# Performance work log

Measured on AMD Instinct MI355X. Metric: run time of the kernel, lower is better.

## Reference

```python
import jax, jax.numpy as jnp
import numpy as np

ALPHA = 0.2  # LeakyReLU negative slope
NEG_BIG = -9e15


def setup_inputs() -> dict:
    key = jax.random.key(0)
    k1, k2, k3, k4 = jax.random.split(key, 4)
    N, F_IN, F_OUT = 8192, 256, 128
    h = jax.random.normal(k1, (N, F_IN), dtype=jnp.float32)
    adj = jax.random.randint(k2, (N, N), 0, 2, dtype=jnp.int32)
    # xavier_uniform with gain=1.414
    def xavier(k, shape, gain=1.414):
        fan_in, fan_out = shape[0], shape[1]
        bound = gain * np.sqrt(6.0 / (fan_in + fan_out))
        return jax.random.uniform(k, shape, jnp.float32, -bound, bound)
    W = xavier(k3, (F_IN, F_OUT))
    a = xavier(k4, (2 * F_OUT, 1))
    return {"h": h, "adj": adj, "W": W, "a": a}


def reference(h, adj, W, a):
    # Wh: [N, F_out]
    Wh = h @ W
    F_out = W.shape[1]
    a1 = a[:F_out, 0]   # attends to source (row) node
    a2 = a[F_out:, 0]   # attends to target (col) node
    # Additive decomposition of concat([Wh_i, Wh_j]) @ a:
    # e[i, j] = leaky_relu(Wh_i . a1 + Wh_j . a2)
    f1 = Wh @ a1  # [N]
    f2 = Wh @ a2  # [N]
    e = jax.nn.leaky_relu(f1[:, None] + f2[None, :], negative_slope=ALPHA)  # [N, N]
    scores = jnp.where(adj > 0, e, jnp.float32(NEG_BIG))
    attention = jax.nn.softmax(scores, axis=1)
    # dropout is identity in eval mode (training=False)
    h_prime = attention @ Wh  # [N, F_out]
    return h_prime
```

## Files before the change

### kernel.cpp

```cpp
#include <hip/hip_runtime.h>


#define N_NODES 8192
#define F_IN 256
#define F_OUT 128
#define RPB 64
#define JCH 128
#define JSPLIT 4
#define JRANGE (N_NODES / JSPLIT)
#define NCH (JRANGE / JCH)

typedef _Float16 half8 __attribute__((ext_vector_type(8)));
typedef float floatx4 __attribute__((ext_vector_type(4)));
typedef float f32x4 __attribute__((ext_vector_type(4)));
typedef int i32x4 __attribute__((ext_vector_type(4)));

__device__ __align__(16) float g_Wh[N_NODES * F_OUT];
__device__ __align__(16) _Float16 g_WhT[(size_t)F_OUT * N_NODES];
__device__ __align__(16) float g_f1[N_NODES];
__device__ __align__(16) float g_f2[N_NODES];
__device__ __align__(16) float g_part[JSPLIT][N_NODES * F_OUT];
__device__ __align__(16) float g_spart[JSPLIT][N_NODES];

__global__ __launch_bounds__(256, 2) void wh_kernel(
    const float* __restrict__ h, const float* __restrict__ W) {
  __shared__ float hT[F_IN][20];
  const int t = threadIdx.x;
  const int i0 = blockIdx.x * 16;
  {
    const int row = t >> 4;
    const int fu = t & 15;
#pragma unroll
    for (int r = 0; r < 4; ++r) {
      const int ku = r * 16 + fu;
      const float4 v = *(const float4*)(h + (size_t)(i0 + row) * F_IN + ku * 4);
      hT[ku * 4 + 0][row] = v.x; hT[ku * 4 + 1][row] = v.y;
      hT[ku * 4 + 2][row] = v.z; hT[ku * 4 + 3][row] = v.w;
    }
  }
  __syncthreads();
  const int c = t & 127;
  const int rg = t >> 7;
  float acc[8];
#pragma unroll
  for (int r = 0; r < 8; ++r) acc[r] = 0.f;
#pragma unroll 8
  for (int k = 0; k < F_IN; ++k) {
    const float wv = W[k * F_OUT + c];
    const float4 x0 = *(const float4*)(&hT[k][rg * 8]);
    const float4 x1 = *(const float4*)(&hT[k][rg * 8 + 4]);
    acc[0] = fmaf(x0.x, wv, acc[0]); acc[1] = fmaf(x0.y, wv, acc[1]);
    acc[2] = fmaf(x0.z, wv, acc[2]); acc[3] = fmaf(x0.w, wv, acc[3]);
    acc[4] = fmaf(x1.x, wv, acc[4]); acc[5] = fmaf(x1.y, wv, acc[5]);
    acc[6] = fmaf(x1.z, wv, acc[6]); acc[7] = fmaf(x1.w, wv, acc[7]);
  }
#pragma unroll
  for (int r = 0; r < 8; ++r)
    g_Wh[(size_t)(i0 + rg * 8 + r) * F_OUT + c] = acc[r];
  union { _Float16 hh[8]; uint4 u4; } pk;
#pragma unroll
  for (int r = 0; r < 8; ++r) pk.hh[r] = (_Float16)acc[r];
  *(uint4*)(g_WhT + (size_t)c * N_NODES + i0 + rg * 8) = pk.u4;
}

__global__ __launch_bounds__(256) void f12_kernel(const float* __restrict__ a) {
  const int t = threadIdx.x;
  const int row = blockIdx.x * 2 + (t >> 7);
  const int c = t & 127;
  const float wh = g_Wh[(size_t)row * F_OUT + c];
  float p1 = wh * a[c];
  float p2 = wh * a[F_OUT + c];
  for (int o = 32; o > 0; o >>= 1) {
    p1 += __shfl_down(p1, o, 64);
    p2 += __shfl_down(p2, o, 64);
  }
  __shared__ float s1[4], s2[4];
  const int w = t >> 6;
  if ((t & 63) == 0) { s1[w] = p1; s2[w] = p2; }
  __syncthreads();
  if ((t & 127) == 0) {
    g_f1[row] = s1[w] + s1[w + 1];
    g_f2[row] = s2[w] + s2[w + 1];
  }
}

__device__ __forceinline__ float score_p(int a, float f2v, float f1r) {
  float s = f1r + f2v;
  s = fmaxf(s, 0.2f * s);
  float arg = (a > 0) ? fmaf(s, 1.44269504088896f, -16.0f) : -1.0e5f;
  return __builtin_amdgcn_exp2f(arg);
}

__global__ __launch_bounds__(256, 2) void gat_attn_kernel(const int* __restrict__ adj) {
  const int t = threadIdx.x;
  const int wave = t >> 6;
  const int lane = t & 63;
  const int mrow = lane & 15;
  const int quad = lane >> 4;
  const int i0 = blockIdx.x * RPB;
  const int js = blockIdx.y;
  const int jbase = js * JRANGE;
  const int jloc = wave * 32 + quad * 8;

  float f1r[4];
#pragma unroll
  for (int tl = 0; tl < 4; ++tl) f1r[tl] = g_f1[i0 + tl * 16 + mrow];

  half8 ones;
#pragma unroll
  for (int e = 0; e < 8; ++e) ones[e] = (_Float16)1;

  floatx4 acc[4][8];
  floatx4 asum[4];
#pragma unroll
  for (int tl = 0; tl < 4; ++tl) {
    asum[tl] = (floatx4)0.f;
#pragma unroll
    for (int ct = 0; ct < 8; ++ct) acc[tl][ct] = (floatx4)0.f;
  }

#pragma unroll 1
  for (int c = 0; c < NCH; ++c) {
    const int jglob = jbase + c * JCH + jloc;

    half8 bfr[8];
#pragma unroll
    for (int ct = 0; ct < 8; ++ct)
      bfr[ct] = *(const half8*)(g_WhT + (size_t)(ct * 16 + mrow) * N_NODES + jglob);
    const float4 F0 = *(const float4*)(g_f2 + jglob);
    const float4 F1 = *(const float4*)(g_f2 + jglob + 4);
    i32x4 A0[4], A1[4];
#pragma unroll
    for (int tl = 0; tl < 4; ++tl) {
      const int* ap = adj + (size_t)(i0 + tl * 16 + mrow) * N_NODES + jglob;
      A0[tl] = __builtin_nontemporal_load((const i32x4*)ap);
      A1[tl] = __builtin_nontemporal_load((const i32x4*)ap + 1);
    }

#pragma unroll
    for (int tl = 0; tl < 4; ++tl) {
      half8 af;
      af[0] = (_Float16)score_p(A0[tl][0], F0.x, f1r[tl]);
      af[1] = (_Float16)score_p(A0[tl][1], F0.y, f1r[tl]);
      af[2] = (_Float16)score_p(A0[tl][2], F0.z, f1r[tl]);
      af[3] = (_Float16)score_p(A0[tl][3], F0.w, f1r[tl]);
      af[4] = (_Float16)score_p(A1[tl][0], F1.x, f1r[tl]);
      af[5] = (_Float16)score_p(A1[tl][1], F1.y, f1r[tl]);
      af[6] = (_Float16)score_p(A1[tl][2], F1.z, f1r[tl]);
      af[7] = (_Float16)score_p(A1[tl][3], F1.w, f1r[tl]);
#pragma unroll
      for (int ct = 0; ct < 8; ++ct)
        acc[tl][ct] = __builtin_amdgcn_mfma_f32_16x16x32_f16(af, bfr[ct], acc[tl][ct], 0, 0, 0);
      asum[tl] = __builtin_amdgcn_mfma_f32_16x16x32_f16(af, ones, asum[tl], 0, 0, 0);
    }
  }

  __shared__ float ldsO[RPB][F_OUT];
  __shared__ float ldsS[4][RPB];

  if (mrow == 0) {
#pragma unroll
    for (int tl = 0; tl < 4; ++tl)
#pragma unroll
      for (int r = 0; r < 4; ++r)
        ldsS[wave][tl * 16 + quad * 4 + r] = asum[tl][r];
  }
  for (int w = 0; w < 4; ++w) {
    if (wave == w) {
#pragma unroll
      for (int tl = 0; tl < 4; ++tl)
#pragma unroll
        for (int ct = 0; ct < 8; ++ct)
#pragma unroll
          for (int r = 0; r < 4; ++r) {
            float* p = &ldsO[tl * 16 + quad * 4 + r][ct * 16 + mrow];
            if (w == 0) *p = acc[tl][ct][r];
            else        *p += acc[tl][ct][r];
          }
    }
    __syncthreads();
  }
  {
    const int row = t >> 2;
    const int c0 = (t & 3) * 32;
    float* dst = g_part[js] + (size_t)(i0 + row) * F_OUT + c0;
#pragma unroll
    for (int q = 0; q < 8; ++q)
      *(f32x4*)(dst + q * 4) = *(const f32x4*)(&ldsO[row][c0 + q * 4]);
    if ((t & 3) == 0)
      g_spart[js][i0 + row] = ldsS[0][row] + ldsS[1][row] +
                              ldsS[2][row] + ldsS[3][row];
  }
}

__global__ __launch_bounds__(256) void comb_kernel(float* __restrict__ out) {
  const int u = blockIdx.x * 256 + threadIdx.x;
  const int row = u >> 5;
  float s = 0.f;
  f32x4 v = (f32x4)0.f;
#pragma unroll
  for (int p = 0; p < JSPLIT; ++p) {
    s += g_spart[p][row];
    v += ((const f32x4*)g_part[p])[u];
  }
  ((f32x4*)out)[u] = v * (1.0f / s);
}

extern "C" void kernel_launch(void* const* d_in, const int* in_sizes, int n_in,
                              void* d_out, int out_size, void* d_ws, size_t ws_size,
                              hipStream_t stream) {
  const float* h = (const float*)d_in[0];
  const int* adj = (const int*)d_in[1];
  const float* W = (const float*)d_in[2];
  const float* a = (const float*)d_in[3];
  float* out = (float*)d_out;
  (void)d_ws; (void)ws_size;

  wh_kernel<<<dim3(N_NODES / 16), dim3(256), 0, stream>>>(h, W);
  f12_kernel<<<dim3(N_NODES / 2), dim3(256), 0, stream>>>(a);
  gat_attn_kernel<<<dim3(N_NODES / RPB, JSPLIT), dim3(256), 0, stream>>>(adj);
  comb_kernel<<<dim3(N_NODES * F_OUT / 4 / 256), dim3(256), 0, stream>>>(out);
}
```

Before: 435.5 us.

## Halve rows per block, halve j-split, and double-buffer adjacency prefetch

Each attention block now handles 32 rows instead of 64, and the j dimension is split 2 ways instead of 4. The grid stays at 512 blocks, but each block walks twice as many j-chunks. The adjacency and f2 loads for the next chunk are issued before the current chunk is computed, so memory latency can overlap the MFMA work. With fewer row tiles, register pressure drops and the combine kernel reads half as many partials. The trade-off is that each WhT fragment is reused across fewer rows, so WhT traffic per output roughly doubles.

After: 456.3 us. +4.8%, slower.

```diff
diff --git a/kernel.cpp b/kernel.cpp
--- a/kernel.cpp
+++ b/kernel.cpp
@@ -4,9 +4,9 @@
 #define N_NODES 8192
 #define F_IN 256
 #define F_OUT 128
-#define RPB 64
+#define RPB 32
 #define JCH 128
-#define JSPLIT 4
+#define JSPLIT 2
 #define JRANGE (N_NODES / JSPLIT)
 #define NCH (JRANGE / JCH)
 
@@ -102,57 +102,69 @@
   const int jbase = js * JRANGE;
   const int jloc = wave * 32 + quad * 8;
 
-  float f1r[4];
-#pragma unroll
-  for (int tl = 0; tl < 4; ++tl) f1r[tl] = g_f1[i0 + tl * 16 + mrow];
+  const float f1r0 = g_f1[i0 + mrow];
+  const float f1r1 = g_f1[i0 + 16 + mrow];
 
   half8 ones;
 #pragma unroll
   for (int e = 0; e < 8; ++e) ones[e] = (_Float16)1;
 
-  floatx4 acc[4][8];
-  floatx4 asum[4];
-#pragma unroll
-  for (int tl = 0; tl < 4; ++tl) {
+  floatx4 acc[2][8];
+  floatx4 asum[2];
+#pragma unroll
+  for (int tl = 0; tl < 2; ++tl) {
     asum[tl] = (floatx4)0.f;
 #pragma unroll
     for (int ct = 0; ct < 8; ++ct) acc[tl][ct] = (floatx4)0.f;
   }
 
-#pragma unroll 1
+  const int* ap0 = adj + (size_t)(i0 + mrow) * N_NODES + jbase + jloc;
+  const int* ap1 = adj + (size_t)(i0 + 16 + mrow) * N_NODES + jbase + jloc;
+
+  i32x4 A0[2][2], A1[2][2];
+  f32x4 Fb[2][2];
+  A0[0][0] = __builtin_nontemporal_load((const i32x4*)ap0);
+  A0[0][1] = __builtin_nontemporal_load((const i32x4*)ap0 + 1);
+  A1[0][0] = __builtin_nontemporal_load((const i32x4*)ap1);
+  A1[0][1] = __builtin_nontemporal_load((const i32x4*)ap1 + 1);
+  Fb[0][0] = *(const f32x4*)(g_f2 + jbase + jloc);
+  Fb[0][1] = *(const f32x4*)(g_f2 + jbase + jloc + 4);
+
+#pragma unroll 2
   for (int c = 0; c < NCH; ++c) {
+    const int b = c & 1, nb = b ^ 1;
     const int jglob = jbase + c * JCH + jloc;
 
     half8 bfr[8];
 #pragma unroll
     for (int ct = 0; ct < 8; ++ct)
       bfr[ct] = *(const half8*)(g_WhT + (size_t)(ct * 16 + mrow) * N_NODES + jglob);
-    const float4 F0 = *(const float4*)(g_f2 + jglob);
-    const float4 F1 = *(const float4*)(g_f2 + jglob + 4);
-    i32x4 A0[4], A1[4];
-#pragma unroll
-    for (int tl = 0; tl < 4; ++tl) {
-      const int* ap = adj + (size_t)(i0 + tl * 16 + mrow) * N_NODES + jglob;
-      A0[tl] = __builtin_nontemporal_load((const i32x4*)ap);
-      A1[tl] = __builtin_nontemporal_load((const i32x4*)ap + 1);
-    }
-
-#pragma unroll
-    for (int tl = 0; tl < 4; ++tl) {
-      half8 af;
-      af[0] = (_Float16)score_p(A0[tl][0], F0.x, f1r[tl]);
-      af[1] = (_Float16)score_p(A0[tl][1], F0.y, f1r[tl]);
-      af[2] = (_Float16)score_p(A0[tl][2], F0.z, f1r[tl]);
-      af[3] = (_Float16)score_p(A0[tl][3], F0.w, f1r[tl]);
-      af[4] = (_Float16)score_p(A1[tl][0], F1.x, f1r[tl]);
-      af[5] = (_Float16)score_p(A1[tl][1], F1.y, f1r[tl]);
-      af[6] = (_Float16)score_p(A1[tl][2], F1.z, f1r[tl]);
-      af[7] = (_Float16)score_p(A1[tl][3], F1.w, f1r[tl]);
-#pragma unroll
-      for (int ct = 0; ct < 8; ++ct)
-        acc[tl][ct] = __builtin_amdgcn_mfma_f32_16x16x32_f16(af, bfr[ct], acc[tl][ct], 0, 0, 0);
-      asum[tl] = __builtin_amdgcn_mfma_f32_16x16x32_f16(af, ones, asum[tl], 0, 0, 0);
-    }
+
+    if (c + 1 < NCH) {
+      A0[nb][0] = __builtin_nontemporal_load((const i32x4*)(ap0 + (c + 1) * JCH));
+      A0[nb][1] = __builtin_nontemporal_load((const i32x4*)(ap0 + (c + 1) * JCH) + 1);
+      A1[nb][0] = __builtin_nontemporal_load((const i32x4*)(ap1 + (c + 1) * JCH));
+      A1[nb][1] = __builtin_nontemporal_load((const i32x4*)(ap1 + (c + 1) * JCH) + 1);
+      Fb[nb][0] = *(const f32x4*)(g_f2 + jglob + JCH);
+      Fb[nb][1] = *(const f32x4*)(g_f2 + jglob + JCH + 4);
+    }
+
+    half8 af0, af1;
+#pragma unroll
+    for (int e = 0; e < 4; ++e) {
+      af0[e]     = (_Float16)score_p(A0[b][0][e], Fb[b][0][e], f1r0);
+      af0[4 + e] = (_Float16)score_p(A0[b][1][e], Fb[b][1][e], f1r0);
+      af1[e]     = (_Float16)score_p(A1[b][0][e], Fb[b][0][e], f1r1);
+      af1[4 + e] = (_Float16)score_p(A1[b][1][e], Fb[b][1][e], f1r1);
+    }
+
+#pragma unroll
+    for (int ct = 0; ct < 8; ++ct) {
+      acc[0][ct] = __builtin_amdgcn_mfma_f32_16x16x32_f16(af0, bfr[ct], acc[0][ct], 0, 0, 0);
+      acc[1][ct] = __builtin_amdgcn_mfma_f32_16x16x32_f16(af1, bfr[ct], acc[1][ct], 0, 0, 0);
+    }
+    asum[0] = __builtin_amdgcn_mfma_f32_16x16x32_f16(af0, ones, asum[0], 0, 0, 0);
+    asum[1] = __builtin_amdgcn_mfma_f32_16x16x32_f16(af1, ones, asum[1], 0, 0, 0);
   }
 
   __shared__ float ldsO[RPB][F_OUT];
@@ -160,7 +172,7 @@
 
   if (mrow == 0) {
 #pragma unroll
-    for (int tl = 0; tl < 4; ++tl)
+    for (int tl = 0; tl < 2; ++tl)
 #pragma unroll
       for (int r = 0; r < 4; ++r)
         ldsS[wave][tl * 16 + quad * 4 + r] = asum[tl][r];
@@ -168,7 +180,7 @@
   for (int w = 0; w < 4; ++w) {
     if (wave == w) {
 #pragma unroll
-      for (int tl = 0; tl < 4; ++tl)
+      for (int tl = 0; tl < 2; ++tl)
 #pragma unroll
         for (int ct = 0; ct < 8; ++ct)
 #pragma unroll
@@ -181,13 +193,13 @@
     __syncthreads();
   }
   {
-    const int row = t >> 2;
-    const int c0 = (t & 3) * 32;
+    const int row = t >> 3;
+    const int c0 = (t & 7) * 16;
     float* dst = g_part[js] + (size_t)(i0 + row) * F_OUT + c0;
 #pragma unroll
-    for (int q = 0; q < 8; ++q)
+    for (int q = 0; q < 4; ++q)
       *(f32x4*)(dst + q * 4) = *(const f32x4*)(&ldsO[row][c0 + q * 4]);
-    if ((t & 3) == 0)
+    if ((t & 7) == 0)
       g_spart[js][i0 + row] = ldsS[0][row] + ldsS[1][row] +
                               ldsS[2][row] + ldsS[3][row];
   }
@@ -196,13 +208,8 @@
 __global__ __launch_bounds__(256) void comb_kernel(float* __restrict__ out) {
   const int u = blockIdx.x * 256 + threadIdx.x;
   const int row = u >> 5;
-  float s = 0.f;
-  f32x4 v = (f32x4)0.f;
-#pragma unroll
-  for (int p = 0; p < JSPLIT; ++p) {
-    s += g_spart[p][row];
-    v += ((const f32x4*)g_part[p])[u];
-  }
+  const float s = g_spart[0][row] + g_spart[1][row];
+  const f32x4 v = ((const f32x4*)g_part[0])[u] + ((const f32x4*)g_part[1])[u];
   ((f32x4*)out)[u] = v * (1.0f / s);
 }
 
```
